# Performance work log

Measured on AMD Instinct MI355X. Metric: run time of the kernel, lower is better.

## Reference

```python
import jax, jax.numpy as jnp
import numpy as np

VOCAB, EMB, WIN = 32000, 300, 5
H1, H2, NY, NZ = 300, 300, 128, 128
B, S = 32, 512


def setup_inputs() -> dict:
    key = jax.random.key(0)
    ks = jax.random.split(key, 16)
    sc = 0.05
    inp = {
        "x": jax.random.randint(ks[0], (B, S, WIN), 0, VOCAB),
        "emb": jax.random.normal(ks[1], (VOCAB, EMB), jnp.float32) * sc,
        "W_ih1": jax.random.normal(ks[2], (H1, EMB * WIN), jnp.float32) * sc,
        "W_hh1": jax.random.normal(ks[3], (H1, H1), jnp.float32) * sc,
        "b_ih1": jax.random.normal(ks[4], (H1,), jnp.float32) * sc,
        "b_hh1": jax.random.normal(ks[5], (H1,), jnp.float32) * sc,
        "W_ih2": jax.random.normal(ks[6], (H2, H1), jnp.float32) * sc,
        "W_hh2": jax.random.normal(ks[7], (H2, H2), jnp.float32) * sc,
        "b_ih2": jax.random.normal(ks[8], (H2,), jnp.float32) * sc,
        "b_hh2": jax.random.normal(ks[9], (H2,), jnp.float32) * sc,
        "fc1_w": jax.random.normal(ks[10], (NY, H1), jnp.float32) * sc,
        "fc1_b": jax.random.normal(ks[11], (NY,), jnp.float32) * sc,
        "fc2_w": jax.random.normal(ks[12], (NZ, H2), jnp.float32) * sc,
        "fc2_b": jax.random.normal(ks[13], (NZ,), jnp.float32) * sc,
    }
    return inp


def reference(x, emb, W_ih1, W_hh1, b_ih1, b_hh1, W_ih2, W_hh2, b_ih2, b_hh2,
              fc1_w, fc1_b, fc2_w, fc2_b):
    b, s, w = x.shape
    xe = emb[jnp.transpose(x, (1, 0, 2))].reshape(s, b, w * emb.shape[1])
    xe = jax.nn.relu(xe)

    h1_0 = jnp.zeros((b, W_hh1.shape[0]), xe.dtype)
    h2_0 = jnp.zeros((b, W_hh2.shape[0]), xe.dtype)

    def step(carry, xt):
        h1, h2 = carry
        h1 = jnp.tanh(xt @ W_ih1.T + b_ih1 + h1 @ W_hh1.T + b_hh1)
        h2 = jnp.tanh(h1 @ W_ih2.T + b_ih2 + h2 @ W_hh2.T + b_hh2)
        return (h1, h2), (h1, h2)

    _, (out1, out2) = jax.lax.scan(step, (h1_0, h2_0), xe)  # [S,B,H]

    out1 = jnp.transpose(out1, (1, 0, 2)).reshape(b * s, -1)
    out2 = jnp.transpose(out2, (1, 0, 2)).reshape(b * s, -1)
    out1 = out1 @ fc1_w.T + fc1_b
    out2 = out2 @ fc2_w.T + fc2_b
    return (out1, out2)
```

## Files before the change

### kernel.cpp

```cpp
#include <hip/hip_runtime.h>
#include <hip/hip_fp16.h>

#define S_LEN 512
#define BATCH 32
#define CHUNK 16

typedef _Float16 hv2  __attribute__((ext_vector_type(2)));
typedef _Float16 half8 __attribute__((ext_vector_type(8)));
typedef float    f32x4 __attribute__((ext_vector_type(4)));

__device__ __forceinline__ float dot2f(hv2 a, hv2 b, float c) {
#if __has_builtin(__builtin_amdgcn_fdot2)
    return __builtin_amdgcn_fdot2(a, b, c, false);
#else
    return c + (float)a.x * (float)b.x + (float)a.y * (float)b.y;
#endif
}

__device__ __forceinline__ float fast_tanh(float x) {
    float e = __expf(2.f * x);
    return 1.f - 2.f / (e + 1.f);
}

#define E8   1280000
#define W18  64000
#define FF8  5120
#define PREP_TOTAL8 (E8 + W18 + FF8 + FF8)

__global__ __launch_bounds__(256) void k_prep(
    const float* __restrict__ emb,  const float* __restrict__ Wih1,
    const float* __restrict__ fc1w, const float* __restrict__ fc2w,
    _Float16* __restrict__ embf, _Float16* __restrict__ Wf1,
    _Float16* __restrict__ F1,   _Float16* __restrict__ F2,
    unsigned int* __restrict__ flags)
{
    int gid = blockIdx.x * 256 + threadIdx.x;
    if (gid < 64) flags[gid] = 0u;
    if (gid >= PREP_TOTAL8) return;

    half8 v;
    _Float16* dst;

    if (gid < E8) {
        int row = gid / 40, c8 = (gid - row * 40) * 8;
        #pragma unroll
        for (int j = 0; j < 8; ++j) {
            int c = c8 + j;
            float f = (c < 300) ? emb[(size_t)row * 300 + c] : 0.f;
            v[j] = (_Float16)(f > 0.f ? f : 0.f);
        }
        dst = embf + (size_t)gid * 8;
    } else if (gid < E8 + W18) {
        int i = gid - E8;
        int row = i / 200, c8 = (i - row * 200) * 8;
        #pragma unroll
        for (int j = 0; j < 8; ++j) {
            int c = c8 + j, w = c / 320, cc = c - w * 320;
            float f = (row < 300 && cc < 300) ? Wih1[(size_t)row * 1500 + w * 300 + cc] : 0.f;
            v[j] = (_Float16)f;
        }
        dst = Wf1 + (size_t)i * 8;
    } else if (gid < E8 + W18 + FF8) {
        int i = gid - E8 - W18;
        int row = i / 40, c8 = (i - row * 40) * 8;
        #pragma unroll
        for (int j = 0; j < 8; ++j) {
            int c = c8 + j;
            v[j] = (_Float16)((c < 300) ? fc1w[(size_t)row * 300 + c] : 0.f);
        }
        dst = F1 + (size_t)i * 8;
    } else {
        int i = gid - E8 - W18 - FF8;
        int row = i / 40, c8 = (i - row * 40) * 8;
        #pragma unroll
        for (int j = 0; j < 8; ++j) {
            int c = c8 + j;
            v[j] = (_Float16)((c < 300) ? fc2w[(size_t)row * 300 + c] : 0.f);
        }
        dst = F2 + (size_t)i * 8;
    }
    *(half8*)dst = v;
}

__global__ __launch_bounds__(256) void k_gemm1_mfma(
    const int* __restrict__ x, const _Float16* __restrict__ embf,
    const _Float16* __restrict__ Wf1, const float* __restrict__ b1,
    const float* __restrict__ b2, float* __restrict__ U)
{
    const int wid  = threadIdx.x >> 6;
    const int lane = threadIdx.x & 63;
    const int m    = lane & 15;
    const int q    = lane >> 4;
    const int r0   = blockIdx.x * 128 + wid * 32;
    const int n0   = blockIdx.y * 160;

    f32x4 acc[2][10];
    #pragma unroll
    for (int i = 0; i < 2; ++i)
        #pragma unroll
        for (int j = 0; j < 10; ++j)
            acc[i][j] = (f32x4){0.f, 0.f, 0.f, 0.f};

    const int rA = r0 + m, rB = r0 + 16 + m;
    const int xbA = ((rA & 31) * S_LEN + (rA >> 5)) * 5;
    const int xbB = ((rB & 31) * S_LEN + (rB >> 5)) * 5;

    for (int w = 0; w < 5; ++w) {
        const int idxA = x[xbA + w];
        const int idxB = x[xbB + w];
        const _Float16* ea = embf + (size_t)idxA * 320;
        const _Float16* eb = embf + (size_t)idxB * 320;
        const _Float16* wb = Wf1 + (size_t)w * 320;
        #pragma unroll
        for (int c = 0; c < 10; ++c) {
            const int k = c * 32 + q * 8;
            half8 a0 = *(const half8*)(ea + k);
            half8 a1 = *(const half8*)(eb + k);
            #pragma unroll
            for (int nt = 0; nt < 10; ++nt) {
                half8 bf = *(const half8*)(wb + (size_t)(n0 + nt * 16 + m) * 1600 + k);
                acc[0][nt] = __builtin_amdgcn_mfma_f32_16x16x32_f16(a0, bf, acc[0][nt], 0, 0, 0);
                acc[1][nt] = __builtin_amdgcn_mfma_f32_16x16x32_f16(a1, bf, acc[1][nt], 0, 0, 0);
            }
        }
    }

    #pragma unroll
    for (int nt = 0; nt < 10; ++nt) {
        const int n = n0 + nt * 16 + m;
        if (n >= 300) continue;
        const float bias = b1[n] + b2[n];
        #pragma unroll
        for (int mt = 0; mt < 2; ++mt) {
            const int rbase = r0 + mt * 16 + q * 4;
            #pragma unroll
            for (int reg = 0; reg < 4; ++reg)
                U[(size_t)(rbase + reg) * 300 + n] = acc[mt][nt][reg] + bias;
        }
    }
}

__global__ __launch_bounds__(256) void k_fc_mfma(
    const _Float16* __restrict__ H1, const _Float16* __restrict__ H2,
    const _Float16* __restrict__ F1, const _Float16* __restrict__ F2,
    const float* __restrict__ fb1, const float* __restrict__ fb2,
    float* __restrict__ out1, float* __restrict__ out2)
{
    const int layer = blockIdx.y;
    const _Float16* H = layer ? H2 : H1;
    const _Float16* F = layer ? F2 : F1;
    const float* bias = layer ? fb2 : fb1;
    float* out        = layer ? out2 : out1;

    const int wid  = threadIdx.x >> 6;
    const int lane = threadIdx.x & 63;
    const int m    = lane & 15;
    const int q    = lane >> 4;
    const int r0   = blockIdx.x * 128 + wid * 32;

    f32x4 acc[2][8];
    #pragma unroll
    for (int i = 0; i < 2; ++i)
        #pragma unroll
        for (int j = 0; j < 8; ++j)
            acc[i][j] = (f32x4){0.f, 0.f, 0.f, 0.f};

    const _Float16* ha = H + (size_t)(r0 + m) * 320;
    const _Float16* hb = H + (size_t)(r0 + 16 + m) * 320;

    #pragma unroll
    for (int c = 0; c < 10; ++c) {
        const int k = c * 32 + q * 8;
        half8 a0 = *(const half8*)(ha + k);
        half8 a1 = *(const half8*)(hb + k);
        #pragma unroll
        for (int nt = 0; nt < 8; ++nt) {
            half8 bf = *(const half8*)(F + (size_t)(nt * 16 + m) * 320 + k);
            acc[0][nt] = __builtin_amdgcn_mfma_f32_16x16x32_f16(a0, bf, acc[0][nt], 0, 0, 0);
            acc[1][nt] = __builtin_amdgcn_mfma_f32_16x16x32_f16(a1, bf, acc[1][nt], 0, 0, 0);
        }
    }

    #pragma unroll
    for (int nt = 0; nt < 8; ++nt) {
        const int n = nt * 16 + m;
        const float bv = bias[n];
        #pragma unroll
        for (int mt = 0; mt < 2; ++mt) {
            #pragma unroll
            for (int reg = 0; reg < 4; ++reg) {
                const int r = r0 + mt * 16 + q * 4 + reg;
                const int oidx = ((r & 31) * S_LEN + (r >> 5)) * 128 + n;
                out[oidx] = acc[mt][nt][reg] + bv;
            }
        }
    }
}

__global__ __launch_bounds__(512, 2) void k_rec_fused(
    const float* __restrict__ U1, const float* __restrict__ Whh1,
    const float* __restrict__ Wih2, const float* __restrict__ Whh2,
    const float* __restrict__ bih2, const float* __restrict__ bhh2,
    _Float16* __restrict__ H1f, _Float16* __restrict__ H2f,
    unsigned int* __restrict__ flags)
{
    const int tid  = threadIdx.x;
    const bool comp = tid < 500;
    const int g    = comp ? tid / 50 : 0;
    const int rt   = comp ? tid % 50 : 0;

    __shared__ __align__(16) _Float16 hbuf[2][320];
    __shared__ float partials[10][304];
    __shared__ __align__(16) _Float16 h1c[CHUNK][320];

    for (int i = tid; i < 2 * 320; i += 512)
        ((_Float16*)hbuf)[i] = (_Float16)0.f;

    if (blockIdx.x < 32) {
        const int b = blockIdx.x;
        hv2 w1[6][16];
        if (comp) {
            #pragma unroll
            for (int i = 0; i < 6; ++i) {
                const float* wr = Whh1 + (size_t)(rt + 50 * i) * 300 + g * 32;
                #pragma unroll
                for (int j = 0; j < 16; ++j) {
                    int c0 = g * 32 + 2 * j;
                    hv2 p;
                    p.x = (c0     < 300) ? (_Float16)wr[2 * j]     : (_Float16)0.f;
                    p.y = (c0 + 1 < 300) ? (_Float16)wr[2 * j + 1] : (_Float16)0.f;
                    w1[i][j] = p;
                }
            }
        }
        __syncthreads();

        float uval = (tid < 300) ? U1[(size_t)b * 300 + tid] : 0.f;

        int cur = 0;
        for (int t = 0; t < S_LEN; ++t) {
            float unext = 0.f;
            if (tid < 300 && t + 1 < S_LEN)
                unext = U1[((size_t)((t + 1) * BATCH + b)) * 300 + tid];

            if (comp) {
                const half8* hp = (const half8*)&hbuf[cur][g * 32];
                float a0 = 0.f, a1 = 0.f, a2 = 0.f, a3 = 0.f, a4 = 0.f, a5 = 0.f;
                #pragma unroll
                for (int jj = 0; jj < 4; ++jj) {
                    half8 q = hp[jj];
                    const hv2* qv = (const hv2*)&q;
                    #pragma unroll
                    for (int j4 = 0; j4 < 4; ++j4) {
                        const int j = 4 * jj + j4;
                        a0 = dot2f(w1[0][j], qv[j4], a0);
                        a1 = dot2f(w1[1][j], qv[j4], a1);
                        a2 = dot2f(w1[2][j], qv[j4], a2);
                        a3 = dot2f(w1[3][j], qv[j4], a3);
                        a4 = dot2f(w1[4][j], qv[j4], a4);
                        a5 = dot2f(w1[5][j], qv[j4], a5);
                    }
                }
                partials[g][rt]       = a0;
                partials[g][rt + 50]  = a1;
                partials[g][rt + 100] = a2;
                partials[g][rt + 150] = a3;
                partials[g][rt + 200] = a4;
                partials[g][rt + 250] = a5;
            }
            __syncthreads();

            if (tid < 300) {
                float s = uval;
                #pragma unroll
                for (int g2 = 0; g2 < 10; ++g2)
                    s += partials[g2][tid];
                float ht = fast_tanh(s);
                _Float16 hf = (_Float16)ht;
                hbuf[cur ^ 1][tid] = hf;
                H1f[((size_t)(t * BATCH + b)) * 320 + tid] = hf;
            } else if (tid < 320) {
                H1f[((size_t)(t * BATCH + b)) * 320 + tid] = (_Float16)0.f;
            }
            __syncthreads();

            if (((t + 1) & (CHUNK - 1)) == 0 && tid == 0) {
                __hip_atomic_store(&flags[b], (unsigned)(t + 1),
                                   __ATOMIC_RELEASE, __HIP_MEMORY_SCOPE_AGENT);
            }
            uval = unext;
            cur ^= 1;
        }
    } else {
        const int b = blockIdx.x - 32;
        hv2 wih[6][16], whh[6][16];
        if (comp) {
            #pragma unroll
            for (int i = 0; i < 6; ++i) {
                const float* wr = Wih2 + (size_t)(rt + 50 * i) * 300 + g * 32;
                const float* wr2 = Whh2 + (size_t)(rt + 50 * i) * 300 + g * 32;
                #pragma unroll
                for (int j = 0; j < 16; ++j) {
                    int c0 = g * 32 + 2 * j;
                    hv2 p, p2;
                    p.x  = (c0     < 300) ? (_Float16)wr[2 * j]      : (_Float16)0.f;
                    p.y  = (c0 + 1 < 300) ? (_Float16)wr[2 * j + 1]  : (_Float16)0.f;
                    p2.x = (c0     < 300) ? (_Float16)wr2[2 * j]     : (_Float16)0.f;
                    p2.y = (c0 + 1 < 300) ? (_Float16)wr2[2 * j + 1] : (_Float16)0.f;
                    wih[i][j] = p;
                    whh[i][j] = p2;
                }
            }
        }
        float bias = 0.f;
        if (tid < 300) bias = bih2[tid] + bhh2[tid];
        __syncthreads();

        int cur = 0;
        for (int t = 0; t < S_LEN; ++t) {
            if ((t & (CHUNK - 1)) == 0) {
                if (tid == 0) {
                    while (__hip_atomic_load(&flags[b], __ATOMIC_ACQUIRE,
                                             __HIP_MEMORY_SCOPE_AGENT) < (unsigned)(t + CHUNK))
                        __builtin_amdgcn_s_sleep(8);
                }
                __syncthreads();
                for (int idx = tid; idx < CHUNK * 40; idx += 512) {
                    int row = idx / 40, o8 = idx - row * 40;
                    *(half8*)&h1c[row][o8 * 8] =
                        *(const half8*)&H1f[((size_t)((t + row) * BATCH + b)) * 320 + o8 * 8];
                }
                __syncthreads();
            }

            if (comp) {
                const half8* h1p = (const half8*)&h1c[t & (CHUNK - 1)][g * 32];
                const half8* h2p = (const half8*)&hbuf[cur][g * 32];
                float a0 = 0.f, a1 = 0.f, a2 = 0.f, a3 = 0.f, a4 = 0.f, a5 = 0.f;
                #pragma unroll
                for (int jj = 0; jj < 4; ++jj) {
                    half8 q1 = h1p[jj];
                    half8 q2 = h2p[jj];
                    const hv2* q1v = (const hv2*)&q1;
                    const hv2* q2v = (const hv2*)&q2;
                    #pragma unroll
                    for (int j4 = 0; j4 < 4; ++j4) {
                        const int j = 4 * jj + j4;
                        a0 = dot2f(wih[0][j], q1v[j4], a0);
                        a1 = dot2f(wih[1][j], q1v[j4], a1);
                        a2 = dot2f(wih[2][j], q1v[j4], a2);
                        a3 = dot2f(wih[3][j], q1v[j4], a3);
                        a4 = dot2f(wih[4][j], q1v[j4], a4);
                        a5 = dot2f(wih[5][j], q1v[j4], a5);
                        a0 = dot2f(whh[0][j], q2v[j4], a0);
                        a1 = dot2f(whh[1][j], q2v[j4], a1);
                        a2 = dot2f(whh[2][j], q2v[j4], a2);
                        a3 = dot2f(whh[3][j], q2v[j4], a3);
                        a4 = dot2f(whh[4][j], q2v[j4], a4);
                        a5 = dot2f(whh[5][j], q2v[j4], a5);
                    }
                }
                partials[g][rt]       = a0;
                partials[g][rt + 50]  = a1;
                partials[g][rt + 100] = a2;
                partials[g][rt + 150] = a3;
                partials[g][rt + 200] = a4;
                partials[g][rt + 250] = a5;
            }
            __syncthreads();

            if (tid < 300) {
                float s = bias;
                #pragma unroll
                for (int g2 = 0; g2 < 10; ++g2)
                    s += partials[g2][tid];
                float ht = fast_tanh(s);
                _Float16 hf = (_Float16)ht;
                hbuf[cur ^ 1][tid] = hf;
                H2f[((size_t)(t * BATCH + b)) * 320 + tid] = hf;
            } else if (tid < 320) {
                H2f[((size_t)(t * BATCH + b)) * 320 + tid] = (_Float16)0.f;
            }
            __syncthreads();
            cur ^= 1;
        }
    }
}

extern "C" void kernel_launch(void* const* d_in, const int* in_sizes, int n_in,
                              void* d_out, int out_size, void* d_ws, size_t ws_size,
                              hipStream_t stream) {
    const int*   x     = (const int*)d_in[0];
    const float* emb   = (const float*)d_in[1];
    const float* Wih1  = (const float*)d_in[2];
    const float* Whh1  = (const float*)d_in[3];
    const float* bih1  = (const float*)d_in[4];
    const float* bhh1  = (const float*)d_in[5];
    const float* Wih2  = (const float*)d_in[6];
    const float* Whh2  = (const float*)d_in[7];
    const float* bih2  = (const float*)d_in[8];
    const float* bhh2  = (const float*)d_in[9];
    const float* fc1w  = (const float*)d_in[10];
    const float* fc1b  = (const float*)d_in[11];
    const float* fc2w  = (const float*)d_in[12];
    const float* fc2b  = (const float*)d_in[13];

    float* out1 = (float*)d_out;
    float* out2 = out1 + (size_t)16384 * 128;

    char* w = (char*)d_ws;
    float*        U1    = (float*)w;
    _Float16*     H1    = (_Float16*)(w + 19660800);
    _Float16*     Wf1   = (_Float16*)(w + 30146560);
    _Float16*     F1    = (_Float16*)(w + 31170560);
    _Float16*     F2    = (_Float16*)(w + 31252480);
    unsigned int* flags = (unsigned int*)(w + 31334400);
    _Float16*     EMBF  = (_Float16*)(w + 31334656);
    _Float16*     H2    = EMBF;

    const int prep_blocks = (PREP_TOTAL8 + 255) / 256;
    k_prep<<<prep_blocks, 256, 0, stream>>>(emb, Wih1, fc1w, fc2w,
                                            EMBF, Wf1, F1, F2, flags);

    dim3 g(128, 2);
    k_gemm1_mfma<<<g, 256, 0, stream>>>(x, EMBF, Wf1, bih1, bhh1, U1);
    k_rec_fused<<<64, 512, 0, stream>>>(U1, Whh1, Wih2, Whh2, bih2, bhh2,
                                        H1, H2, flags);
    k_fc_mfma<<<g, 256, 0, stream>>>(H1, H2, F1, F2, fc1b, fc2b, out1, out2);
}
```

Baseline: 907.8 us.

## Hoist layer-2 input projection into per-chunk MFMA and batch hidden-state stores

Layer-2 blocks now compute W_ih2·h1 for a whole 16-step chunk at once with MFMA instructions, using a new fp16 copy of W_ih2 made in the prep kernel. Only the W_hh2 matvec stays inside the sequential step loop, which halves that block's per-step dot-product work and register footprint. Both layers now keep the chunk's hidden states in LDS and write them to global memory once per chunk instead of every step. Layer 1 also stages U1 for the chunk into LDS from registers prefetched one chunk ahead. Plain __syncthreads are replaced with LDS-only waitcnt barriers, at the cost of a dynamic LDS allocation and an extra chunk-level GEMM phase that adds latency before each chunk's recurrence.

```diff
diff --git a/kernel.cpp b/kernel.cpp
--- a/kernel.cpp
+++ b/kernel.cpp
@@ -22,17 +22,26 @@
     return 1.f - 2.f / (e + 1.f);
 }
 
+__device__ __forceinline__ void lds_barrier() {
+    __asm__ volatile("s_waitcnt lgkmcnt(0)\n\ts_barrier" ::: "memory");
+}
+__device__ __forceinline__ void vm_drain() {
+    __asm__ volatile("s_waitcnt vmcnt(0)" ::: "memory");
+}
+
 #define E8   1280000
 #define W18  64000
+#define W28  12800
 #define FF8  5120
-#define PREP_TOTAL8 (E8 + W18 + FF8 + FF8)
+#define PREP_TOTAL8 (E8 + W18 + W28 + FF8 + FF8)
 
 __global__ __launch_bounds__(256) void k_prep(
     const float* __restrict__ emb,  const float* __restrict__ Wih1,
-    const float* __restrict__ fc1w, const float* __restrict__ fc2w,
+    const float* __restrict__ Wih2, const float* __restrict__ fc1w,
+    const float* __restrict__ fc2w,
     _Float16* __restrict__ embf, _Float16* __restrict__ Wf1,
-    _Float16* __restrict__ F1,   _Float16* __restrict__ F2,
-    unsigned int* __restrict__ flags)
+    _Float16* __restrict__ Wf2,  _Float16* __restrict__ F1,
+    _Float16* __restrict__ F2,   unsigned int* __restrict__ flags)
 {
     int gid = blockIdx.x * 256 + threadIdx.x;
     if (gid < 64) flags[gid] = 0u;
@@ -60,8 +69,18 @@
             v[j] = (_Float16)f;
         }
         dst = Wf1 + (size_t)i * 8;
-    } else if (gid < E8 + W18 + FF8) {
+    } else if (gid < E8 + W18 + W28) {
         int i = gid - E8 - W18;
+        int row = i / 40, c8 = (i - row * 40) * 8;
+        #pragma unroll
+        for (int j = 0; j < 8; ++j) {
+            int c = c8 + j;
+            float f = (row < 300 && c < 300) ? Wih2[(size_t)row * 300 + c] : 0.f;
+            v[j] = (_Float16)f;
+        }
+        dst = Wf2 + (size_t)i * 8;
+    } else if (gid < E8 + W18 + W28 + FF8) {
+        int i = gid - E8 - W18 - W28;
         int row = i / 40, c8 = (i - row * 40) * 8;
         #pragma unroll
         for (int j = 0; j < 8; ++j) {
@@ -70,7 +89,7 @@
         }
         dst = F1 + (size_t)i * 8;
     } else {
-        int i = gid - E8 - W18 - FF8;
+        int i = gid - E8 - W18 - W28 - FF8;
         int row = i / 40, c8 = (i - row * 40) * 8;
         #pragma unroll
         for (int j = 0; j < 8; ++j) {
@@ -197,24 +216,42 @@
     }
 }
 
-__global__ __launch_bounds__(512, 2) void k_rec_fused(
+#define LDS_BYTES 52096
+
+__device__ __forceinline__ void load_u_regs(float* up, const float* __restrict__ U1,
+                                            int b, int t0) {
+    #pragma unroll
+    for (int j = 0; j < 10; ++j) {
+        int e = threadIdx.x + 512 * j;
+        int row = e / 300, col = e - row * 300;
+        up[j] = (e < 4800) ? U1[((size_t)((t0 + row) * BATCH + b)) * 300 + col] : 0.f;
+    }
+}
+
+__global__ __launch_bounds__(512) void k_rec_fused(
     const float* __restrict__ U1, const float* __restrict__ Whh1,
-    const float* __restrict__ Wih2, const float* __restrict__ Whh2,
+    const _Float16* __restrict__ Wf2, const float* __restrict__ Whh2,
     const float* __restrict__ bih2, const float* __restrict__ bhh2,
     _Float16* __restrict__ H1f, _Float16* __restrict__ H2f,
     unsigned int* __restrict__ flags)
 {
+    extern __shared__ char smem[];
+    float   (*partials)[304] = (float(*)[304])smem;
+    _Float16 (*hc)[320]      = (_Float16(*)[320])(smem + 12160);
+    float   (*uc)[304]       = (float(*)[304])(smem + 22400);
+    _Float16 (*h1s)[320]     = (_Float16(*)[320])(smem + 41856);
+
     const int tid  = threadIdx.x;
     const bool comp = tid < 500;
     const int g    = comp ? tid / 50 : 0;
     const int rt   = comp ? tid % 50 : 0;
-
-    __shared__ __align__(16) _Float16 hbuf[2][320];
-    __shared__ float partials[10][304];
-    __shared__ __align__(16) _Float16 h1c[CHUNK][320];
-
-    for (int i = tid; i < 2 * 320; i += 512)
-        ((_Float16*)hbuf)[i] = (_Float16)0.f;
+    const int lane = tid & 63;
+    const int wid  = tid >> 6;
+    const int lm   = lane & 15;
+    const int lq   = lane >> 4;
+
+    for (int i = tid; i < CHUNK * 320; i += 512)
+        ((_Float16*)hc)[i] = (_Float16)0.f;
 
     if (blockIdx.x < 32) {
         const int b = blockIdx.x;
@@ -233,156 +270,190 @@
                 }
             }
         }
-        __syncthreads();
-
-        float uval = (tid < 300) ? U1[(size_t)b * 300 + tid] : 0.f;
-
-        int cur = 0;
-        for (int t = 0; t < S_LEN; ++t) {
-            float unext = 0.f;
-            if (tid < 300 && t + 1 < S_LEN)
-                unext = U1[((size_t)((t + 1) * BATCH + b)) * 300 + tid];
-
-            if (comp) {
-                const half8* hp = (const half8*)&hbuf[cur][g * 32];
-                float a0 = 0.f, a1 = 0.f, a2 = 0.f, a3 = 0.f, a4 = 0.f, a5 = 0.f;
-                #pragma unroll
-                for (int jj = 0; jj < 4; ++jj) {
-                    half8 q = hp[jj];
-                    const hv2* qv = (const hv2*)&q;
+
+        float upref[10];
+        load_u_regs(upref, U1, b, 0);
+
+        for (int c = 0; c < 32; ++c) {
+            const int t0 = c * CHUNK;
+            if (c > 0) {
+                const int tb = t0 - CHUNK;
+                for (int i = tid; i < CHUNK * 40; i += 512) {
+                    int row = i / 40, c8 = i - row * 40;
+                    half8 v = *(const half8*)&hc[row][c8 * 8];
+                    *(half8*)&H1f[((size_t)((tb + row) * BATCH + b)) * 320 + c8 * 8] = v;
+                }
+            }
+            #pragma unroll
+            for (int j = 0; j < 10; ++j) {
+                int e = tid + 512 * j;
+                if (e < 4800) {
+                    int row = e / 300, col = e - row * 300;
+                    uc[row][col] = upref[j];
+                }
+            }
+            if (c > 0) {
+                vm_drain();
+                if (tid == 0)
+                    __hip_atomic_store(&flags[b], (unsigned)t0,
+                                       __ATOMIC_RELEASE, __HIP_MEMORY_SCOPE_AGENT);
+            }
+            if (c + 1 < 32)
+                load_u_regs(upref, U1, b, t0 + CHUNK);
+            lds_barrier();
+
+            for (int s = 0; s < CHUNK; ++s) {
+                if (comp) {
+                    const half8* hp = (const half8*)&hc[(s - 1) & 15][g * 32];
+                    float a0 = 0.f, a1 = 0.f, a2 = 0.f, a3 = 0.f, a4 = 0.f, a5 = 0.f;
                     #pragma unroll
-                    for (int j4 = 0; j4 < 4; ++j4) {
-                        const int j = 4 * jj + j4;
-                        a0 = dot2f(w1[0][j], qv[j4], a0);
-                        a1 = dot2f(w1[1][j], qv[j4], a1);
-                        a2 = dot2f(w1[2][j], qv[j4], a2);
-                        a3 = dot2f(w1[3][j], qv[j4], a3);
-                        a4 = dot2f(w1[4][j], qv[j4], a4);
-                        a5 = dot2f(w1[5][j], qv[j4], a5);
+                    for (int jj = 0; jj < 4; ++jj) {
+                        half8 q8 = hp[jj];
+                        const hv2* qv = (const hv2*)&q8;
+                        #pragma unroll
+                        for (int j4 = 0; j4 < 4; ++j4) {
+                            const int j = 4 * jj + j4;
+                            a0 = dot2f(w1[0][j], qv[j4], a0);
+                            a1 = dot2f(w1[1][j], qv[j4], a1);
+                            a2 = dot2f(w1[2][j], qv[j4], a2);
+                            a3 = dot2f(w1[3][j], qv[j4], a3);
+                            a4 = dot2f(w1[4][j], qv[j4], a4);
+                            a5 = dot2f(w1[5][j], qv[j4], a5);
+                        }
                     }
-                }
-                partials[g][rt]       = a0;
-                partials[g][rt + 50]  = a1;
-                partials[g][rt + 100] = a2;
-                partials[g][rt + 150] = a3;
-                partials[g][rt + 200] = a4;
-                partials[g][rt + 250] = a5;
-            }
-            __syncthreads();
-
-            if (tid < 300) {
-                float s = uval;
-                #pragma unroll
-                for (int g2 = 0; g2 < 10; ++g2)
-                    s += partials[g2][tid];
-                float ht = fast_tanh(s);
-                _Float16 hf = (_Float16)ht;
-                hbuf[cur ^ 1][tid] = hf;
-                H1f[((size_t)(t * BATCH + b)) * 320 + tid] = hf;
-            } else if (tid < 320) {
-                H1f[((size_t)(t * BATCH + b)) * 320 + tid] = (_Float16)0.f;
-            }
-            __syncthreads();
-
-            if (((t + 1) & (CHUNK - 1)) == 0 && tid == 0) {
-                __hip_atomic_store(&flags[b], (unsigned)(t + 1),
+                    partials[g][rt]       = a0;
+                    partials[g][rt + 50]  = a1;
+                    partials[g][rt + 100] = a2;
+                    partials[g][rt + 150] = a3;
+                    partials[g][rt + 200] = a4;
+                    partials[g][rt + 250] = a5;
+                }
+                lds_barrier();
+                if (tid < 300) {
+                    float ssum = uc[s][tid];
+                    #pragma unroll
+                    for (int g2 = 0; g2 < 10; ++g2)
+                        ssum += partials[g2][tid];
+                    hc[s][tid] = (_Float16)fast_tanh(ssum);
+                }
+                lds_barrier();
+            }
+        }
+        {
+            const int tb = S_LEN - CHUNK;
+            for (int i = tid; i < CHUNK * 40; i += 512) {
+                int row = i / 40, c8 = i - row * 40;
+                half8 v = *(const half8*)&hc[row][c8 * 8];
+                *(half8*)&H1f[((size_t)((tb + row) * BATCH + b)) * 320 + c8 * 8] = v;
+            }
+            vm_drain();
+            if (tid == 0)
+                __hip_atomic_store(&flags[b], (unsigned)S_LEN,
                                    __ATOMIC_RELEASE, __HIP_MEMORY_SCOPE_AGENT);
-            }
-            uval = unext;
-            cur ^= 1;
         }
     } else {
         const int b = blockIdx.x - 32;
-        hv2 wih[6][16], whh[6][16];
+        hv2 whh[6][16];
         if (comp) {
             #pragma unroll
             for (int i = 0; i < 6; ++i) {
-                const float* wr = Wih2 + (size_t)(rt + 50 * i) * 300 + g * 32;
-                const float* wr2 = Whh2 + (size_t)(rt + 50 * i) * 300 + g * 32;
+                const float* wr = Whh2 + (size_t)(rt + 50 * i) * 300 + g * 32;
                 #pragma unroll
                 for (int j = 0; j < 16; ++j) {
                     int c0 = g * 32 + 2 * j;
-                    hv2 p, p2;
-                    p.x  = (c0     < 300) ? (_Float16)wr[2 * j]      : (_Float16)0.f;
-                    p.y  = (c0 + 1 < 300) ? (_Float16)wr[2 * j + 1]  : (_Float16)0.f;
-                    p2.x = (c0     < 300) ? (_Float16)wr2[2 * j]     : (_Float16)0.f;
-                    p2.y = (c0 + 1 < 300) ? (_Float16)wr2[2 * j + 1] : (_Float16)0.f;
-                    wih[i][j] = p;
-                    whh[i][j] = p2;
-                }
-            }
-        }
-        float bias = 0.f;
-        if (tid < 300) bias = bih2[tid] + bhh2[tid];
-        __syncthreads();
-
-        int cur = 0;
-        for (int t = 0; t < S_LEN; ++t) {
-            if ((t & (CHUNK - 1)) == 0) {
-                if (tid == 0) {
-                    while (__hip_atomic_load(&flags[b], __ATOMIC_ACQUIRE,
-                                             __HIP_MEMORY_SCOPE_AGENT) < (unsigned)(t + CHUNK))
-                        __builtin_amdgcn_s_sleep(8);
-                }
-                __syncthreads();
-                for (int idx = tid; idx < CHUNK * 40; idx += 512) {
-                    int row = idx / 40, o8 = idx - row * 40;
-                    *(half8*)&h1c[row][o8 * 8] =
-                        *(const half8*)&H1f[((size_t)((t + row) * BATCH + b)) * 320 + o8 * 8];
-                }
-                __syncthreads();
-            }
-
-            if (comp) {
-                const half8* h1p = (const half8*)&h1c[t & (CHUNK - 1)][g * 32];
-                const half8* h2p = (const half8*)&hbuf[cur][g * 32];
-                float a0 = 0.f, a1 = 0.f, a2 = 0.f, a3 = 0.f, a4 = 0.f, a5 = 0.f;
+                    hv2 p;
+                    p.x = (c0     < 300) ? (_Float16)wr[2 * j]     : (_Float16)0.f;
+                    p.y = (c0 + 1 < 300) ? (_Float16)wr[2 * j + 1] : (_Float16)0.f;
+                    whh[i][j] = p;
+                }
+            }
+        }
+        float bias = (tid < 300) ? (bih2[tid] + bhh2[tid]) : 0.f;
+
+        for (int c = 0; c < 32; ++c) {
+            const int t0 = c * CHUNK;
+            if (c > 0) {
+                const int tb = t0 - CHUNK;
+                for (int i = tid; i < CHUNK * 40; i += 512) {
+                    int row = i / 40, c8 = i - row * 40;
+                    half8 v = *(const half8*)&hc[row][c8 * 8];
+                    *(half8*)&H2f[((size_t)((tb + row) * BATCH + b)) * 320 + c8 * 8] = v;
+                }
+            }
+            if (tid == 0) {
+                while (__hip_atomic_load(&flags[b], __ATOMIC_ACQUIRE,
+                                         __HIP_MEMORY_SCOPE_AGENT) < (unsigned)(t0 + CHUNK))
+                    __builtin_amdgcn_s_sleep(2);
+            }
+            __syncthreads();
+
+            for (int i = tid; i < CHUNK * 40; i += 512) {
+                int row = i / 40, c8 = i - row * 40;
+                *(half8*)&h1s[row][c8 * 8] =
+                    *(const half8*)&H1f[((size_t)((t0 + row) * BATCH + b)) * 320 + c8 * 8];
+            }
+            lds_barrier();
+
+            for (int nt = wid; nt < 19; nt += 8) {
+                f32x4 acc = (f32x4){0.f, 0.f, 0.f, 0.f};
+                const int n = nt * 16 + lm;
+                const _Float16* wrow = Wf2 + (size_t)n * 320;
                 #pragma unroll
-                for (int jj = 0; jj < 4; ++jj) {
-                    half8 q1 = h1p[jj];
-                    half8 q2 = h2p[jj];
-                    const hv2* q1v = (const hv2*)&q1;
-                    const hv2* q2v = (const hv2*)&q2;
+                for (int k0 = 0; k0 < 320; k0 += 32) {
+                    half8 a  = *(const half8*)&h1s[lm][k0 + lq * 8];
+                    half8 bf = *(const half8*)&wrow[k0 + lq * 8];
+                    acc = __builtin_amdgcn_mfma_f32_16x16x32_f16(a, bf, acc, 0, 0, 0);
+                }
+                #pragma unroll
+                for (int reg = 0; reg < 4; ++reg)
+                    uc[lq * 4 + reg][n] = acc[reg];
+            }
+            lds_barrier();
+
+            for (int s = 0; s < CHUNK; ++s) {
+                if (comp) {
+                    const half8* hp = (const half8*)&hc[(s - 1) & 15][g * 32];
+                    float a0 = 0.f, a1 = 0.f, a2 = 0.f, a3 = 0.f, a4 = 0.f, a5 = 0.f;
                     #pragma unroll
-                    for (int j4 = 0; j4 < 4; ++j4) {
-                        const int j = 4 * jj + j4;
-                        a0 = dot2f(wih[0][j], q1v[j4], a0);
-                        a1 = dot2f(wih[1][j], q1v[j4], a1);
-                        a2 = dot2f(wih[2][j], q1v[j4], a2);
-                        a3 = dot2f(wih[3][j], q1v[j4], a3);
-                        a4 = dot2f(wih[4][j], q1v[j4], a4);
-                        a5 = dot2f(wih[5][j], q1v[j4], a5);
-                        a0 = dot2f(whh[0][j], q2v[j4], a0);
-                        a1 = dot2f(whh[1][j], q2v[j4], a1);
-                        a2 = dot2f(whh[2][j], q2v[j4], a2);
-                        a3 = dot2f(whh[3][j], q2v[j4], a3);
-                        a4 = dot2f(whh[4][j], q2v[j4], a4);
-                        a5 = dot2f(whh[5][j], q2v[j4], a5);
+                    for (int jj = 0; jj < 4; ++jj) {
+                        half8 q8 = hp[jj];
+                        const hv2* qv = (const hv2*)&q8;
+                        #pragma unroll
+                        for (int j4 = 0; j4 < 4; ++j4) {
+                            const int j = 4 * jj + j4;
+                            a0 = dot2f(whh[0][j], qv[j4], a0);
+                            a1 = dot2f(whh[1][j], qv[j4], a1);
+                            a2 = dot2f(whh[2][j], qv[j4], a2);
+                            a3 = dot2f(whh[3][j], qv[j4], a3);
+                            a4 = dot2f(whh[4][j], qv[j4], a4);
+                            a5 = dot2f(whh[5][j], qv[j4], a5);
+                        }
                     }
-                }
-                partials[g][rt]       = a0;
-                partials[g][rt + 50]  = a1;
-                partials[g][rt + 100] = a2;
-                partials[g][rt + 150] = a3;
-                partials[g][rt + 200] = a4;
-                partials[g][rt + 250] = a5;
-            }
-            __syncthreads();
-
-            if (tid < 300) {
-                float s = bias;
-                #pragma unroll
-                for (int g2 = 0; g2 < 10; ++g2)
-                    s += partials[g2][tid];
-                float ht = fast_tanh(s);
-                _Float16 hf = (_Float16)ht;
-                hbuf[cur ^ 1][tid] = hf;
-                H2f[((size_t)(t * BATCH + b)) * 320 + tid] = hf;
-            } else if (tid < 320) {
-                H2f[((size_t)(t * BATCH + b)) * 320 + tid] = (_Float16)0.f;
-            }
-            __syncthreads();
-            cur ^= 1;
+                    partials[g][rt]       = a0;
+                    partials[g][rt + 50]  = a1;
+                    partials[g][rt + 100] = a2;
+                    partials[g][rt + 150] = a3;
+                    partials[g][rt + 200] = a4;
+                    partials[g][rt + 250] = a5;
+                }
+                lds_barrier();
+                if (tid < 300) {
+                    float ssum = bias + uc[s][tid];
+                    #pragma unroll
+                    for (int g2 = 0; g2 < 10; ++g2)
+                        ssum += partials[g2][tid];
+                    hc[s][tid] = (_Float16)fast_tanh(ssum);
+                }
+                lds_barrier();
+            }
+        }
+        {
+            const int tb = S_LEN - CHUNK;
+            for (int i = tid; i < CHUNK * 40; i += 512) {
+                int row = i / 40, c8 = i - row * 40;
+                half8 v = *(const half8*)&hc[row][c8 * 8];
+                *(half8*)&H2f[((size_t)((tb + row) * BATCH + b)) * 320 + c8 * 8] = v;
+            }
         }
     }
 }
@@ -412,19 +483,20 @@
     float*        U1    = (float*)w;
     _Float16*     H1    = (_Float16*)(w + 19660800);
     _Float16*     Wf1   = (_Float16*)(w + 30146560);
-    _Float16*     F1    = (_Float16*)(w + 31170560);
-    _Float16*     F2    = (_Float16*)(w + 31252480);
-    unsigned int* flags = (unsigned int*)(w + 31334400);
-    _Float16*     EMBF  = (_Float16*)(w + 31334656);
+    _Float16*     Wf2   = (_Float16*)(w + 31170560);
+    _Float16*     F1    = (_Float16*)(w + 31375360);
+    _Float16*     F2    = (_Float16*)(w + 31457280);
+    unsigned int* flags = (unsigned int*)(w + 31539200);
+    _Float16*     EMBF  = (_Float16*)(w + 31539456);
     _Float16*     H2    = EMBF;
 
     const int prep_blocks = (PREP_TOTAL8 + 255) / 256;
-    k_prep<<<prep_blocks, 256, 0, stream>>>(emb, Wih1, fc1w, fc2w,
-                                            EMBF, Wf1, F1, F2, flags);
+    k_prep<<<prep_blocks, 256, 0, stream>>>(emb, Wih1, Wih2, fc1w, fc2w,
+                                            EMBF, Wf1, Wf2, F1, F2, flags);
 
     dim3 g(128, 2);
     k_gemm1_mfma<<<g, 256, 0, stream>>>(x, EMBF, Wf1, bih1, bhh1, U1);
-    k_rec_fused<<<64, 512, 0, stream>>>(U1, Whh1, Wih2, Whh2, bih2, bhh2,
-                                        H1, H2, flags);
+    k_rec_fused<<<64, 512, LDS_BYTES, stream>>>(U1, Whh1, Wf2, Whh2, bih2, bhh2,
+                                                H1, H2, flags);
     k_fc_mfma<<<g, 256, 0, stream>>>(H1, H2, F1, F2, fc1b, fc2b, out1, out2);
 }
```

Result: faster. 846.3 us (-6.8%).
